# Kernel tuning notes

Measured on AMD Instinct MI355X. Metric: run time of the kernel, lower is better.

Reference implementation:

```python
import jax, jax.numpy as jnp
import numpy as np

N = 100000       # nodes
E = 1600000      # edges (avg degree 16)
W_IN = 256
W_HID = 64
T = 4            # node types
K = 10           # diffusion hops (num_layers)
ALPHA = 0.1
EPS = 1e-12


def setup_inputs() -> dict:
    key = jax.random.key(0)
    k1, k2, k3, k4, k5 = jax.random.split(key, 5)
    X = jax.random.normal(k1, (N, W_IN), dtype=jnp.float32)
    W_enc = jax.random.normal(k2, (W_IN, W_HID), dtype=jnp.float32) * 0.1  # xavier-ish scale
    b_enc = jnp.zeros((W_HID,), dtype=jnp.float32)
    gaussian_sample = jax.random.normal(k3, (N * W_HID,), dtype=jnp.float32)
    edge_index = jax.random.randint(k4, (2, E), 0, N, dtype=jnp.int64)
    node_type = jax.random.randint(k5, (N,), 0, T, dtype=jnp.int64)
    return {"X": X, "W_enc": W_enc, "b_enc": b_enc,
            "gaussian_sample": gaussian_sample,
            "edge_index": edge_index, "node_type": node_type}


def _l2_normalize_rows(x):
    # F.normalize(x, p=2, dim=1)
    n = jnp.sqrt(jnp.sum(x * x, axis=1, keepdims=True))
    return x / jnp.maximum(n, EPS)


def reference(X, W_enc, b_enc, gaussian_sample, edge_index, node_type):
    # --- type-aware encoding: Linear + L2 row-normalize (act='l2') ---
    H = X @ W_enc + b_enc                       # [N, W_HID]
    H = _l2_normalize_rows(H)

    # --- per-type statistics (vectorized segment reduce over node types) ---
    counts = jax.ops.segment_sum(jnp.ones((N,), H.dtype), node_type, num_segments=T)  # [T]
    mean_t = jax.ops.segment_sum(H, node_type, num_segments=T) / counts[:, None]      # [T, W_HID]
    dev2 = (H - mean_t[node_type]) ** 2
    # original: 1/sqrt(n_i - 1) * sum((H_i - mean_i)^2)  (sum, not mean — faithful)
    std_t = jax.ops.segment_sum(dev2, node_type, num_segments=T) / jnp.sqrt(counts - 1.0)[:, None]

    tilde_H = (H - mean_t[node_type]) / std_t[node_type]  # [N, W_HID]

    # --- wasserstein loss: W1 between flattened embeddings and a standard gaussian
    # sample of equal size (scipy wasserstein_distance == mean |sorted diffs|).
    # Original detaches embeddings (numpy), so stop_gradient the whole loss.
    emb = jax.lax.stop_gradient(tilde_H).reshape(-1)
    loss = jax.lax.stop_gradient(
        jnp.mean(jnp.abs(jnp.sort(gaussian_sample) - jnp.sort(emb))))

    # dropout with training=False -> identity

    # --- PPR diffusion: K steps of row-normalized SpMM with restart ---
    src, dst = edge_index[0], edge_index[1]
    deg = jax.ops.segment_sum(jnp.ones((E,), H.dtype), dst, num_segments=N)
    deg = jnp.maximum(deg, 1.0)                 # avoid div-by-zero for isolated nodes
    edge_norm = (1.0 / deg)[dst]                # D^{-1} A (row normalization)

    Z = tilde_H
    for _ in range(K):
        agg = jax.ops.segment_sum(Z[src] * edge_norm[:, None], dst, num_segments=N)
        Z = (1.0 - ALPHA) * agg + ALPHA * tilde_H

    # --- de-normalize back with per-type stats, then L2 row-normalize ---
    Z = Z * std_t[node_type] + mean_t[node_type]
    Z = _l2_normalize_rows(Z)
    return (Z, loss)
```

## Files before the change

### kernel.cpp

```cpp
#include <hip/hip_runtime.h>
#include <math.h>

#define WH 64
#define WIN 256
#define TT 4
#define ALPHA_C 0.1f
#define STATS_GRID 256
#define KC 32
#define ENC_T 64
#define ENC_BN 32
#define XTS 36
#define BINS 16384
#define BIN_SCALE 1024.0f
#define HG 256
#define SB 128
#define ST 256

typedef unsigned short ushortT;

__device__ __forceinline__ unsigned pack_bf16(float a, float b) {
  unsigned ua = __float_as_uint(a), ub = __float_as_uint(b);
  ua = (ua + 0x7FFFu + ((ua >> 16) & 1u)) >> 16;
  ub = ((ub + 0x7FFFu + ((ub >> 16) & 1u)) >> 16) << 16;
  return (ua & 0xFFFFu) | ub;
}
__device__ __forceinline__ float bf_lo(unsigned p) { return __uint_as_float(p << 16); }
__device__ __forceinline__ float bf_hi(unsigned p) { return __uint_as_float(p & 0xFFFF0000u); }

__global__ __launch_bounds__(64, 3) void k_encode(const float* __restrict__ X,
                                                  const float* __restrict__ W,
                                                  const float* __restrict__ bias,
                                                  float* __restrict__ H, int N) {
  __shared__ __align__(16) float XsT[KC * XTS];
  __shared__ __align__(16) float Ws[KC * WH];
  int tid = threadIdx.x;
  int ng = tid >> 3, cg = tid & 7;
  int nodeBase = blockIdx.x * ENC_BN;
  float acc[4][8] = {};
  for (int k0 = 0; k0 < WIN; k0 += KC) {
    __syncthreads();
    const float4* Wg4 = (const float4*)(W + (size_t)k0 * WH);
    float4* Ws4 = (float4*)Ws;
#pragma unroll
    for (int j = 0; j < 8; ++j) Ws4[tid + j * 64] = Wg4[tid + j * 64];
#pragma unroll
    for (int i = 0; i < 4; ++i) {
      int idx = tid + i * 64;
      int ln = idx >> 3, f4 = idx & 7;
      int node = nodeBase + ln;
      float4 xv = (node < N)
                      ? *(const float4*)(X + (size_t)node * WIN + k0 + f4 * 4)
                      : make_float4(0.f, 0.f, 0.f, 0.f);
      float* p = &XsT[(f4 * 4) * XTS + ln];
      p[0] = xv.x;
      p[XTS] = xv.y;
      p[2 * XTS] = xv.z;
      p[3 * XTS] = xv.w;
    }
    __syncthreads();
#pragma unroll 8
    for (int k = 0; k < KC; ++k) {
      float4 a0 = *(const float4*)&XsT[k * XTS + ng * 4];
      float4 b0 = *(const float4*)&Ws[k * WH + cg * 8];
      float4 b1 = *(const float4*)&Ws[k * WH + cg * 8 + 4];
      float av[4] = {a0.x, a0.y, a0.z, a0.w};
      float bb[8] = {b0.x, b0.y, b0.z, b0.w, b1.x, b1.y, b1.z, b1.w};
#pragma unroll
      for (int i = 0; i < 4; ++i)
#pragma unroll
        for (int j = 0; j < 8; ++j) acc[i][j] += av[i] * bb[j];
    }
  }
  float4 bb0 = *(const float4*)(bias + cg * 8);
  float4 bb1 = *(const float4*)(bias + cg * 8 + 4);
  float bv[8] = {bb0.x, bb0.y, bb0.z, bb0.w, bb1.x, bb1.y, bb1.z, bb1.w};
#pragma unroll
  for (int i = 0; i < 4; ++i) {
    float h[8];
    float s = 0.f;
#pragma unroll
    for (int j = 0; j < 8; ++j) {
      h[j] = acc[i][j] + bv[j];
      s += h[j] * h[j];
    }
    s += __shfl_xor(s, 1, 64);
    s += __shfl_xor(s, 2, 64);
    s += __shfl_xor(s, 4, 64);
    float r = 1.0f / fmaxf(sqrtf(s), 1e-12f);
    int node = nodeBase + ng * 4 + i;
    if (node < N) {
      float4 o0 = {h[0] * r, h[1] * r, h[2] * r, h[3] * r};
      float4 o1 = {h[4] * r, h[5] * r, h[6] * r, h[7] * r};
      *(float4*)(H + (size_t)node * WH + cg * 8) = o0;
      *(float4*)(H + (size_t)node * WH + cg * 8 + 4) = o1;
    }
  }
}

__global__ __launch_bounds__(256) void k_stats(const float* __restrict__ H,
                                               const int* __restrict__ nt,
                                               float* __restrict__ psum,
                                               float* __restrict__ psq,
                                               float* __restrict__ pcnt, int NW) {
  __shared__ float ls[TT * WH], ls2[TT * WH];
  __shared__ float lc[TT];
  ls[threadIdx.x] = 0.0f;
  ls2[threadIdx.x] = 0.0f;
  if (threadIdx.x < TT) lc[threadIdx.x] = 0.0f;
  __syncthreads();
  for (int i = blockIdx.x * 256 + threadIdx.x; i < NW; i += STATS_GRID * 256) {
    int nn = i >> 6, d = i & 63;
    int t = nt[nn];
    float v = H[i];
    atomicAdd(&ls[t * WH + d], v);
    atomicAdd(&ls2[t * WH + d], v * v);
    if (d == 0) atomicAdd(&lc[t], 1.0f);
  }
  __syncthreads();
  psum[blockIdx.x * 256 + threadIdx.x] = ls[threadIdx.x];
  psq[blockIdx.x * 256 + threadIdx.x] = ls2[threadIdx.x];
  if (threadIdx.x < TT) pcnt[blockIdx.x * TT + threadIdx.x] = lc[threadIdx.x];
}

__global__ __launch_bounds__(256) void k_reduce_stats(const float* __restrict__ psum,
                                                      const float* __restrict__ psq,
                                                      const float* __restrict__ pcnt,
                                                      float* __restrict__ mean,
                                                      float* __restrict__ stdv,
                                                      float* __restrict__ counts) {
  __shared__ float c[TT];
  if (threadIdx.x < TT) {
    float s = 0.0f;
    for (int b = 0; b < STATS_GRID; ++b) s += pcnt[b * TT + threadIdx.x];
    counts[threadIdx.x] = s;
    c[threadIdx.x] = s;
  }
  __syncthreads();
  float s = 0.0f, q = 0.0f;
  for (int b = 0; b < STATS_GRID; ++b) {
    s += psum[b * 256 + threadIdx.x];
    q += psq[b * 256 + threadIdx.x];
  }
  float n = c[threadIdx.x >> 6];
  float m = s / n;
  mean[threadIdx.x] = m;
  stdv[threadIdx.x] = (q - s * s / n) / sqrtf(n - 1.0f);
}

__global__ __launch_bounds__(256) void k_tilde_hist(float* __restrict__ H,
                                                    const int* __restrict__ nt,
                                                    const float* __restrict__ mean,
                                                    const float* __restrict__ stdv,
                                                    ushortT* __restrict__ tb,
                                                    unsigned* __restrict__ pe, int NW) {
  __shared__ unsigned hist[BINS];
  for (int b = threadIdx.x; b < BINS; b += 256) hist[b] = 0;
  __syncthreads();
  for (int i = blockIdx.x * 256 + threadIdx.x; i < NW; i += HG * 256) {
    int nn = i >> 6, d = i & 63;
    int t = nt[nn];
    float v = (H[i] - mean[t * WH + d]) / stdv[t * WH + d];
    H[i] = v;
    unsigned u = __float_as_uint(v);
    tb[i] = (ushortT)((u + 0x7FFFu + ((u >> 16) & 1u)) >> 16);
    int b = (int)((v + 8.0f) * BIN_SCALE);
    b = min(max(b, 0), BINS - 1);
    atomicAdd(&hist[b], 1u);
  }
  __syncthreads();
  for (int b = threadIdx.x; b < BINS; b += 256)
    pe[(size_t)blockIdx.x * BINS + b] = hist[b];
}

__global__ __launch_bounds__(256) void k_histG(const float* __restrict__ g,
                                               unsigned* __restrict__ pg, int M) {
  __shared__ unsigned hist[BINS];
  for (int b = threadIdx.x; b < BINS; b += 256) hist[b] = 0;
  __syncthreads();
  for (int i = blockIdx.x * 256 + threadIdx.x; i < M; i += HG * 256) {
    float v = g[i];
    int b = (int)((v + 8.0f) * BIN_SCALE);
    b = min(max(b, 0), BINS - 1);
    atomicAdd(&hist[b], 1u);
  }
  __syncthreads();
  for (int b = threadIdx.x; b < BINS; b += 256)
    pg[(size_t)blockIdx.x * BINS + b] = hist[b];
}

__global__ __launch_bounds__(256) void k_diff(const unsigned* __restrict__ pg,
                                              const unsigned* __restrict__ pe,
                                              int* __restrict__ diff) {
  int b = blockIdx.x * 256 + threadIdx.x;
  int s = 0;
  for (int p = 0; p < HG; ++p)
    s += (int)pg[(size_t)p * BINS + b] - (int)pe[(size_t)p * BINS + b];
  diff[b] = s;
}

__global__ __launch_bounds__(1024) void k_wass(const int* __restrict__ diff,
                                               float* __restrict__ out, int M, int NW) {
  int tid = threadIdx.x;
  int lo = tid * (BINS / 1024);
  int d[BINS / 1024];
  int s = 0;
#pragma unroll
  for (int i = 0; i < BINS / 1024; ++i) {
    d[i] = diff[lo + i];
    s += d[i];
  }
  __shared__ int sc[1024];
  sc[tid] = s;
  __syncthreads();
  for (int st = 1; st < 1024; st <<= 1) {
    int v = (tid >= st) ? sc[tid - st] : 0;
    __syncthreads();
    sc[tid] += v;
    __syncthreads();
  }
  int run = sc[tid] - s;
  long long a = 0;
#pragma unroll
  for (int i = 0; i < BINS / 1024; ++i) {
    run += d[i];
    a += (long long)(run < 0 ? -run : run);
  }
  __shared__ long long rd[1024];
  rd[tid] = a;
  __syncthreads();
  for (int st = 512; st > 0; st >>= 1) {
    if (tid < st) rd[tid] += rd[tid + st];
    __syncthreads();
  }
  if (tid == 0) out[NW] = (float)((double)rd[0] * (1.0 / (double)BIN_SCALE) / (double)M);
}

__global__ __launch_bounds__(256) void k_degi(const int* __restrict__ dst,
                                              unsigned* __restrict__ degi, int E) {
  int e = blockIdx.x * 256 + threadIdx.x;
  if (e < E) atomicAdd(&degi[dst[e]], 1u);
}

__global__ __launch_bounds__(ST) void k_scan_part(const unsigned* __restrict__ in,
                                                  unsigned* __restrict__ bsum, int L) {
  int C = (L + SB * ST - 1) / (SB * ST);
  int base = (blockIdx.x * ST + threadIdx.x) * C;
  int hi = min(base + C, L);
  unsigned s = 0;
  for (int i = base; i < hi; ++i) s += in[i];
  __shared__ unsigned red[ST];
  red[threadIdx.x] = s;
  __syncthreads();
  for (int st = ST / 2; st > 0; st >>= 1) {
    if (threadIdx.x < st) red[threadIdx.x] += red[threadIdx.x + st];
    __syncthreads();
  }
  if (threadIdx.x == 0) bsum[blockIdx.x] = red[0];
}
__global__ __launch_bounds__(ST) void k_scan_mid(unsigned* __restrict__ bsum) {
  __shared__ unsigned ts[ST];
  unsigned v = (threadIdx.x < SB) ? bsum[threadIdx.x] : 0u;
  ts[threadIdx.x] = v;
  __syncthreads();
  for (int st = 1; st < ST; st <<= 1) {
    unsigned u = (threadIdx.x >= (unsigned)st) ? ts[threadIdx.x - st] : 0u;
    __syncthreads();
    ts[threadIdx.x] += u;
    __syncthreads();
  }
  if (threadIdx.x < SB) bsum[threadIdx.x] = ts[threadIdx.x] - v;
}
__global__ __launch_bounds__(ST) void k_scan_apply(const unsigned* __restrict__ in,
                                                   const unsigned* __restrict__ bsum,
                                                   unsigned* __restrict__ outp, int L) {
  int C = (L + SB * ST - 1) / (SB * ST);
  int base = (blockIdx.x * ST + threadIdx.x) * C;
  int hi = min(base + C, L);
  unsigned s = 0;
  for (int i = base; i < hi; ++i) s += in[i];
  __shared__ unsigned ts[ST];
  ts[threadIdx.x] = s;
  __syncthreads();
  for (int st = 1; st < ST; st <<= 1) {
    unsigned u = (threadIdx.x >= (unsigned)st) ? ts[threadIdx.x - st] : 0u;
    __syncthreads();
    ts[threadIdx.x] += u;
    __syncthreads();
  }
  unsigned run = bsum[blockIdx.x] + ts[threadIdx.x] - s;
  for (int i = base; i < hi; ++i) {
    unsigned c = in[i];
    outp[i] = run;
    run += c;
  }
}

__global__ __launch_bounds__(256) void k_build(const int* __restrict__ src,
                                               const int* __restrict__ dst,
                                               const unsigned* __restrict__ off,
                                               unsigned* __restrict__ cur,
                                               unsigned* __restrict__ esrc, int E) {
  int e = blockIdx.x * 256 + threadIdx.x;
  if (e >= E) return;
  int t = dst[e];
  unsigned p = off[t] + atomicAdd(&cur[t], 1u);
  esrc[p] = (unsigned)src[e];
}

__global__ __launch_bounds__(256) void k_spmm(const unsigned* __restrict__ off,
                                              const unsigned* __restrict__ degi,
                                              const unsigned* __restrict__ esrc,
                                              const ushortT* __restrict__ Zb,
                                              const float* __restrict__ tilde,
                                              ushortT* __restrict__ Zn,
                                              const int* __restrict__ nt,
                                              const float* __restrict__ mean,
                                              const float* __restrict__ stdv,
                                              float* __restrict__ outp,
                                              int fin, int N) {
  int lane = threadIdx.x & 63, wv = threadIdx.x >> 6;
  int j = lane >> 3, c = lane & 7;
  int n = blockIdx.x * 32 + wv * 8 + j;
  if (n >= N) return;
  unsigned st = off[n], dg = degi[n];
  const unsigned* ep = esrc + st;
  float a[8] = {};
  unsigned e = 0;
  for (; e + 4 <= dg; e += 4) {
    unsigned s0 = ep[e], s1 = ep[e + 1], s2 = ep[e + 2], s3 = ep[e + 3];
    uint4 v0 = *((const uint4*)(Zb + (size_t)s0 * WH) + c);
    uint4 v1 = *((const uint4*)(Zb + (size_t)s1 * WH) + c);
    uint4 v2 = *((const uint4*)(Zb + (size_t)s2 * WH) + c);
    uint4 v3 = *((const uint4*)(Zb + (size_t)s3 * WH) + c);
    a[0] += bf_lo(v0.x) + bf_lo(v1.x) + bf_lo(v2.x) + bf_lo(v3.x);
    a[1] += bf_hi(v0.x) + bf_hi(v1.x) + bf_hi(v2.x) + bf_hi(v3.x);
    a[2] += bf_lo(v0.y) + bf_lo(v1.y) + bf_lo(v2.y) + bf_lo(v3.y);
    a[3] += bf_hi(v0.y) + bf_hi(v1.y) + bf_hi(v2.y) + bf_hi(v3.y);
    a[4] += bf_lo(v0.z) + bf_lo(v1.z) + bf_lo(v2.z) + bf_lo(v3.z);
    a[5] += bf_hi(v0.z) + bf_hi(v1.z) + bf_hi(v2.z) + bf_hi(v3.z);
    a[6] += bf_lo(v0.w) + bf_lo(v1.w) + bf_lo(v2.w) + bf_lo(v3.w);
    a[7] += bf_hi(v0.w) + bf_hi(v1.w) + bf_hi(v2.w) + bf_hi(v3.w);
  }
  for (; e < dg; ++e) {
    unsigned s = ep[e];
    uint4 v = *((const uint4*)(Zb + (size_t)s * WH) + c);
    a[0] += bf_lo(v.x); a[1] += bf_hi(v.x);
    a[2] += bf_lo(v.y); a[3] += bf_hi(v.y);
    a[4] += bf_lo(v.z); a[5] += bf_hi(v.z);
    a[6] += bf_lo(v.w); a[7] += bf_hi(v.w);
  }
  float wn = (1.0f - ALPHA_C) / fmaxf((float)dg, 1.0f);
  const float4* Tr = (const float4*)(tilde + (size_t)n * WH);
  float4 t0 = Tr[2 * c], t1 = Tr[2 * c + 1];
  float o0 = wn * a[0] + ALPHA_C * t0.x, o1 = wn * a[1] + ALPHA_C * t0.y;
  float o2 = wn * a[2] + ALPHA_C * t0.z, o3 = wn * a[3] + ALPHA_C * t0.w;
  float o4 = wn * a[4] + ALPHA_C * t1.x, o5 = wn * a[5] + ALPHA_C * t1.y;
  float o6 = wn * a[6] + ALPHA_C * t1.z, o7 = wn * a[7] + ALPHA_C * t1.w;
  if (!fin) {
    uint4 p;
    p.x = pack_bf16(o0, o1);
    p.y = pack_bf16(o2, o3);
    p.z = pack_bf16(o4, o5);
    p.w = pack_bf16(o6, o7);
    *((uint4*)(Zn + (size_t)n * WH) + c) = p;
  } else {
    int t = nt[n];
    float4 m0 = *(const float4*)(mean + t * WH + c * 8);
    float4 m1 = *(const float4*)(mean + t * WH + c * 8 + 4);
    float4 d0 = *(const float4*)(stdv + t * WH + c * 8);
    float4 d1 = *(const float4*)(stdv + t * WH + c * 8 + 4);
    float z0 = o0 * d0.x + m0.x, z1 = o1 * d0.y + m0.y;
    float z2 = o2 * d0.z + m0.z, z3 = o3 * d0.w + m0.w;
    float z4 = o4 * d1.x + m1.x, z5 = o5 * d1.y + m1.y;
    float z6 = o6 * d1.z + m1.z, z7 = o7 * d1.w + m1.w;
    float s = z0 * z0 + z1 * z1 + z2 * z2 + z3 * z3 +
              z4 * z4 + z5 * z5 + z6 * z6 + z7 * z7;
    s += __shfl_xor(s, 1, 64);
    s += __shfl_xor(s, 2, 64);
    s += __shfl_xor(s, 4, 64);
    float r = 1.0f / fmaxf(sqrtf(s), 1e-12f);
    float4 w0 = {z0 * r, z1 * r, z2 * r, z3 * r};
    float4 w1 = {z4 * r, z5 * r, z6 * r, z7 * r};
    *(float4*)(outp + (size_t)n * WH + c * 8) = w0;
    *(float4*)(outp + (size_t)n * WH + c * 8 + 4) = w1;
  }
}

extern "C" void kernel_launch(void* const* d_in, const int* in_sizes, int n_in,
                              void* d_out, int out_size, void* d_ws, size_t ws_size,
                              hipStream_t stream) {
  const float* X = (const float*)d_in[0];
  const float* W = (const float*)d_in[1];
  const float* bias = (const float*)d_in[2];
  const float* g = (const float*)d_in[3];
  const int* ei = (const int*)d_in[4];
  const int* nt = (const int*)d_in[5];

  const int N = in_sizes[5];
  const int E = in_sizes[4] / 2;
  const int M = in_sizes[3];
  const int NW = N * WH;
  const int* srcp = ei;
  const int* dstp = ei + E;

  char* w = (char*)d_ws;
  size_t o = 0;
  auto alloc = [&](size_t bytes) {
    size_t r = o;
    o += (bytes + 255) & ~(size_t)255;
    return r;
  };
  size_t off_stats = alloc(4096);
  size_t off_psum  = alloc((size_t)STATS_GRID * 256 * 4);
  size_t off_psq   = alloc((size_t)STATS_GRID * 256 * 4);
  size_t off_pcnt  = alloc((size_t)STATS_GRID * TT * 4);
  size_t off_diff  = alloc((size_t)BINS * 4);
  size_t off_bsum  = alloc((size_t)SB * 4);
  size_t off_degi  = alloc((size_t)N * 4);
  size_t off_cur   = alloc((size_t)N * 4);
  size_t off_off   = alloc((size_t)N * 4);
  size_t off_esrc  = alloc((size_t)E * 4);
  size_t off_tilde = alloc((size_t)NW * 4);
  size_t off_tbf   = alloc((size_t)NW * 2);
  size_t off_bufA  = alloc((size_t)NW * 4);
  size_t off_bufB  = alloc((size_t)NW * 4);

  float* counts = (float*)(w + off_stats + 0);
  float* mean   = (float*)(w + off_stats + 256);
  float* stdv   = (float*)(w + off_stats + 1280);
  float* psum   = (float*)(w + off_psum);
  float* psq    = (float*)(w + off_psq);
  float* pcnt   = (float*)(w + off_pcnt);
  int* diff     = (int*)(w + off_diff);
  unsigned* bsum = (unsigned*)(w + off_bsum);
  unsigned* degi = (unsigned*)(w + off_degi);
  unsigned* cur  = (unsigned*)(w + off_cur);
  unsigned* offp = (unsigned*)(w + off_off);
  unsigned* esrc = (unsigned*)(w + off_esrc);
  float* tilde   = (float*)(w + off_tilde);
  ushortT* tbf   = (ushortT*)(w + off_tbf);
  unsigned* pg   = (unsigned*)(w + off_bufA);
  unsigned* pe   = (unsigned*)(w + off_bufB);
  ushortT* ZA    = (ushortT*)(w + off_bufA);
  ushortT* ZB    = (ushortT*)(w + off_bufB);
  float* out = (float*)d_out;

  hipMemsetAsync(w + off_degi, 0, off_cur - off_degi + (size_t)N * 4, stream);

  k_encode<<<(N + ENC_BN - 1) / ENC_BN, ENC_T, 0, stream>>>(X, W, bias, tilde, N);

  k_stats<<<STATS_GRID, 256, 0, stream>>>(tilde, nt, psum, psq, pcnt, NW);
  k_reduce_stats<<<1, 256, 0, stream>>>(psum, psq, pcnt, mean, stdv, counts);

  k_tilde_hist<<<HG, 256, 0, stream>>>(tilde, nt, mean, stdv, tbf, pe, NW);
  k_histG<<<HG, 256, 0, stream>>>(g, pg, M);

  k_diff<<<BINS / 256, 256, 0, stream>>>(pg, pe, diff);
  k_wass<<<1, 1024, 0, stream>>>(diff, out, M, NW);

  k_degi<<<(E + 255) / 256, 256, 0, stream>>>(dstp, degi, E);
  k_scan_part<<<SB, ST, 0, stream>>>(degi, bsum, N);
  k_scan_mid<<<1, ST, 0, stream>>>(bsum);
  k_scan_apply<<<SB, ST, 0, stream>>>(degi, bsum, offp, N);
  k_build<<<(E + 255) / 256, 256, 0, stream>>>(srcp, dstp, offp, cur, esrc, E);

  const ushortT* Zc = tbf;
  for (int k = 0; k < 10; ++k) {
    ushortT* Zn = (k & 1) ? ZB : ZA;
    int fin = (k == 9) ? 1 : 0;
    k_spmm<<<(N + 31) / 32, 256, 0, stream>>>(offp, degi, esrc, Zc, tilde, Zn,
                                              nt, mean, stdv, out, fin, N);
    Zc = Zn;
  }
}
```

Measured before the change: 898.7 us.

## Fuse diffusion hops into one cooperative persistent kernel with grid sync

Replaces the ten per-hop SpMM launches with a single cooperative kernel that keeps per-node offsets, degrees and restart features in registers across hops and separates hops with grid.sync. Each thread covers up to four nodes in a strided persistent layout, aiming to remove launch overhead and repeated loads of node metadata. CSR construction also records each edge's rank from the degree-counting atomic, so the build pass needs no second atomic or cursor array. The risks are grid-wide barrier cost, lower occupancy from the fixed 1024x256 grid, and a fallback to the old path if the cooperative launch fails.

```diff
diff --git a/kernel.cpp b/kernel.cpp
--- a/kernel.cpp
+++ b/kernel.cpp
@@ -1,5 +1,8 @@
 #include <hip/hip_runtime.h>
+#include <hip/hip_cooperative_groups.h>
 #include <math.h>
+
+namespace cg = cooperative_groups;
 
 #define WH 64
 #define WIN 256
@@ -15,6 +18,9 @@
 #define HG 256
 #define SB 128
 #define ST 256
+#define HOP_B 1024
+#define HOP_T 256
+#define HOP_S ((HOP_B * HOP_T) / 8)
 
 typedef unsigned short ushortT;
 
@@ -34,7 +40,7 @@
   __shared__ __align__(16) float XsT[KC * XTS];
   __shared__ __align__(16) float Ws[KC * WH];
   int tid = threadIdx.x;
-  int ng = tid >> 3, cg = tid & 7;
+  int ng = tid >> 3, cg_ = tid & 7;
   int nodeBase = blockIdx.x * ENC_BN;
   float acc[4][8] = {};
   for (int k0 = 0; k0 < WIN; k0 += KC) {
@@ -61,8 +67,8 @@
 #pragma unroll 8
     for (int k = 0; k < KC; ++k) {
       float4 a0 = *(const float4*)&XsT[k * XTS + ng * 4];
-      float4 b0 = *(const float4*)&Ws[k * WH + cg * 8];
-      float4 b1 = *(const float4*)&Ws[k * WH + cg * 8 + 4];
+      float4 b0 = *(const float4*)&Ws[k * WH + cg_ * 8];
+      float4 b1 = *(const float4*)&Ws[k * WH + cg_ * 8 + 4];
       float av[4] = {a0.x, a0.y, a0.z, a0.w};
       float bb[8] = {b0.x, b0.y, b0.z, b0.w, b1.x, b1.y, b1.z, b1.w};
 #pragma unroll
@@ -71,8 +77,8 @@
         for (int j = 0; j < 8; ++j) acc[i][j] += av[i] * bb[j];
     }
   }
-  float4 bb0 = *(const float4*)(bias + cg * 8);
-  float4 bb1 = *(const float4*)(bias + cg * 8 + 4);
+  float4 bb0 = *(const float4*)(bias + cg_ * 8);
+  float4 bb1 = *(const float4*)(bias + cg_ * 8 + 4);
   float bv[8] = {bb0.x, bb0.y, bb0.z, bb0.w, bb1.x, bb1.y, bb1.z, bb1.w};
 #pragma unroll
   for (int i = 0; i < 4; ++i) {
@@ -91,8 +97,8 @@
     if (node < N) {
       float4 o0 = {h[0] * r, h[1] * r, h[2] * r, h[3] * r};
       float4 o1 = {h[4] * r, h[5] * r, h[6] * r, h[7] * r};
-      *(float4*)(H + (size_t)node * WH + cg * 8) = o0;
-      *(float4*)(H + (size_t)node * WH + cg * 8 + 4) = o1;
+      *(float4*)(H + (size_t)node * WH + cg_ * 8) = o0;
+      *(float4*)(H + (size_t)node * WH + cg_ * 8 + 4) = o1;
     }
   }
 }
@@ -235,10 +241,21 @@
   if (tid == 0) out[NW] = (float)((double)rd[0] * (1.0 / (double)BIN_SCALE) / (double)M);
 }
 
-__global__ __launch_bounds__(256) void k_degi(const int* __restrict__ dst,
-                                              unsigned* __restrict__ degi, int E) {
+__global__ __launch_bounds__(256) void k_degi_rank(const int* __restrict__ dst,
+                                                   unsigned* __restrict__ degi,
+                                                   unsigned* __restrict__ rank, int E) {
   int e = blockIdx.x * 256 + threadIdx.x;
-  if (e < E) atomicAdd(&degi[dst[e]], 1u);
+  if (e < E) rank[e] = atomicAdd(&degi[dst[e]], 1u);
+}
+
+__global__ __launch_bounds__(256) void k_build2(const int* __restrict__ src,
+                                                const int* __restrict__ dst,
+                                                const unsigned* __restrict__ off,
+                                                const unsigned* __restrict__ rank,
+                                                unsigned* __restrict__ esrc, int E) {
+  int e = blockIdx.x * 256 + threadIdx.x;
+  if (e >= E) return;
+  esrc[off[dst[e]] + rank[e]] = (unsigned)src[e];
 }
 
 __global__ __launch_bounds__(ST) void k_scan_part(const unsigned* __restrict__ in,
@@ -295,16 +312,111 @@
   }
 }
 
-__global__ __launch_bounds__(256) void k_build(const int* __restrict__ src,
-                                               const int* __restrict__ dst,
-                                               const unsigned* __restrict__ off,
-                                               unsigned* __restrict__ cur,
-                                               unsigned* __restrict__ esrc, int E) {
-  int e = blockIdx.x * 256 + threadIdx.x;
-  if (e >= E) return;
-  int t = dst[e];
-  unsigned p = off[t] + atomicAdd(&cur[t], 1u);
-  esrc[p] = (unsigned)src[e];
+__global__ __launch_bounds__(HOP_T, 4) void k_hops(
+    const unsigned* __restrict__ off, const unsigned* __restrict__ degi,
+    const unsigned* __restrict__ esrc, const ushortT* __restrict__ Z0,
+    const float* __restrict__ tilde, ushortT* __restrict__ ZAp,
+    ushortT* __restrict__ ZBp, const int* __restrict__ nt,
+    const float* __restrict__ mean, const float* __restrict__ stdv,
+    float* __restrict__ outp, int N, int K) {
+  cg::grid_group grid = cg::this_grid();
+  int g = blockIdx.x * HOP_T + threadIdx.x;
+  int slot = g >> 3, c = g & 7;
+  unsigned stv[4], dgv[4];
+  float4 tA[4], tB[4];
+  int nn[4];
+#pragma unroll
+  for (int i = 0; i < 4; ++i) {
+    int n = slot + i * HOP_S;
+    nn[i] = -1;
+    stv[i] = 0; dgv[i] = 0;
+    tA[i] = make_float4(0.f, 0.f, 0.f, 0.f);
+    tB[i] = make_float4(0.f, 0.f, 0.f, 0.f);
+    if (n < N) {
+      nn[i] = n;
+      stv[i] = off[n];
+      dgv[i] = degi[n];
+      const float4* Tr = (const float4*)(tilde + (size_t)n * WH);
+      tA[i] = Tr[2 * c];
+      tB[i] = Tr[2 * c + 1];
+    }
+  }
+  const ushortT* Zb = Z0;
+  ushortT* Zn = ZAp;
+  for (int k = 0; k < K; ++k) {
+    int fin = (k == K - 1);
+#pragma unroll
+    for (int i = 0; i < 4; ++i) {
+      if (nn[i] < 0) break;
+      int n = nn[i];
+      const unsigned* ep = esrc + stv[i];
+      unsigned dg = dgv[i];
+      float a[8] = {};
+      unsigned e = 0;
+      for (; e + 4 <= dg; e += 4) {
+        unsigned s0 = ep[e], s1 = ep[e + 1], s2 = ep[e + 2], s3 = ep[e + 3];
+        uint4 v0 = *((const uint4*)(Zb + (size_t)s0 * WH) + c);
+        uint4 v1 = *((const uint4*)(Zb + (size_t)s1 * WH) + c);
+        uint4 v2 = *((const uint4*)(Zb + (size_t)s2 * WH) + c);
+        uint4 v3 = *((const uint4*)(Zb + (size_t)s3 * WH) + c);
+        a[0] += bf_lo(v0.x) + bf_lo(v1.x) + bf_lo(v2.x) + bf_lo(v3.x);
+        a[1] += bf_hi(v0.x) + bf_hi(v1.x) + bf_hi(v2.x) + bf_hi(v3.x);
+        a[2] += bf_lo(v0.y) + bf_lo(v1.y) + bf_lo(v2.y) + bf_lo(v3.y);
+        a[3] += bf_hi(v0.y) + bf_hi(v1.y) + bf_hi(v2.y) + bf_hi(v3.y);
+        a[4] += bf_lo(v0.z) + bf_lo(v1.z) + bf_lo(v2.z) + bf_lo(v3.z);
+        a[5] += bf_hi(v0.z) + bf_hi(v1.z) + bf_hi(v2.z) + bf_hi(v3.z);
+        a[6] += bf_lo(v0.w) + bf_lo(v1.w) + bf_lo(v2.w) + bf_lo(v3.w);
+        a[7] += bf_hi(v0.w) + bf_hi(v1.w) + bf_hi(v2.w) + bf_hi(v3.w);
+      }
+      for (; e < dg; ++e) {
+        unsigned s = ep[e];
+        uint4 v = *((const uint4*)(Zb + (size_t)s * WH) + c);
+        a[0] += bf_lo(v.x); a[1] += bf_hi(v.x);
+        a[2] += bf_lo(v.y); a[3] += bf_hi(v.y);
+        a[4] += bf_lo(v.z); a[5] += bf_hi(v.z);
+        a[6] += bf_lo(v.w); a[7] += bf_hi(v.w);
+      }
+      float wn = (1.0f - ALPHA_C) / fmaxf((float)dg, 1.0f);
+      float o0 = wn * a[0] + ALPHA_C * tA[i].x, o1 = wn * a[1] + ALPHA_C * tA[i].y;
+      float o2 = wn * a[2] + ALPHA_C * tA[i].z, o3 = wn * a[3] + ALPHA_C * tA[i].w;
+      float o4 = wn * a[4] + ALPHA_C * tB[i].x, o5 = wn * a[5] + ALPHA_C * tB[i].y;
+      float o6 = wn * a[6] + ALPHA_C * tB[i].z, o7 = wn * a[7] + ALPHA_C * tB[i].w;
+      if (!fin) {
+        uint4 p;
+        p.x = pack_bf16(o0, o1);
+        p.y = pack_bf16(o2, o3);
+        p.z = pack_bf16(o4, o5);
+        p.w = pack_bf16(o6, o7);
+        *((uint4*)(Zn + (size_t)n * WH) + c) = p;
+      } else {
+        int t = nt[n];
+        float4 m0 = *(const float4*)(mean + t * WH + c * 8);
+        float4 m1 = *(const float4*)(mean + t * WH + c * 8 + 4);
+        float4 d0 = *(const float4*)(stdv + t * WH + c * 8);
+        float4 d1 = *(const float4*)(stdv + t * WH + c * 8 + 4);
+        float z0 = o0 * d0.x + m0.x, z1 = o1 * d0.y + m0.y;
+        float z2 = o2 * d0.z + m0.z, z3 = o3 * d0.w + m0.w;
+        float z4 = o4 * d1.x + m1.x, z5 = o5 * d1.y + m1.y;
+        float z6 = o6 * d1.z + m1.z, z7 = o7 * d1.w + m1.w;
+        float s = z0 * z0 + z1 * z1 + z2 * z2 + z3 * z3 +
+                  z4 * z4 + z5 * z5 + z6 * z6 + z7 * z7;
+        s += __shfl_xor(s, 1, 64);
+        s += __shfl_xor(s, 2, 64);
+        s += __shfl_xor(s, 4, 64);
+        float r = 1.0f / fmaxf(sqrtf(s), 1e-12f);
+        float4 w0 = {z0 * r, z1 * r, z2 * r, z3 * r};
+        float4 w1 = {z4 * r, z5 * r, z6 * r, z7 * r};
+        *(float4*)(outp + (size_t)n * WH + c * 8) = w0;
+        *(float4*)(outp + (size_t)n * WH + c * 8 + 4) = w1;
+      }
+    }
+    if (k < K - 1) {
+      __threadfence();
+      grid.sync();
+      Zb = Zn;
+      Zn = (Zn == ZAp) ? ZBp : ZAp;
+    }
+  }
 }
 
 __global__ __launch_bounds__(256) void k_spmm(const unsigned* __restrict__ off,
@@ -417,7 +529,6 @@
   size_t off_diff  = alloc((size_t)BINS * 4);
   size_t off_bsum  = alloc((size_t)SB * 4);
   size_t off_degi  = alloc((size_t)N * 4);
-  size_t off_cur   = alloc((size_t)N * 4);
   size_t off_off   = alloc((size_t)N * 4);
   size_t off_esrc  = alloc((size_t)E * 4);
   size_t off_tilde = alloc((size_t)NW * 4);
@@ -434,18 +545,18 @@
   int* diff     = (int*)(w + off_diff);
   unsigned* bsum = (unsigned*)(w + off_bsum);
   unsigned* degi = (unsigned*)(w + off_degi);
-  unsigned* cur  = (unsigned*)(w + off_cur);
   unsigned* offp = (unsigned*)(w + off_off);
   unsigned* esrc = (unsigned*)(w + off_esrc);
   float* tilde   = (float*)(w + off_tilde);
   ushortT* tbf   = (ushortT*)(w + off_tbf);
   unsigned* pg   = (unsigned*)(w + off_bufA);
   unsigned* pe   = (unsigned*)(w + off_bufB);
+  unsigned* rank = (unsigned*)(w + off_bufB);
   ushortT* ZA    = (ushortT*)(w + off_bufA);
   ushortT* ZB    = (ushortT*)(w + off_bufB);
   float* out = (float*)d_out;
 
-  hipMemsetAsync(w + off_degi, 0, off_cur - off_degi + (size_t)N * 4, stream);
+  hipMemsetAsync(w + off_degi, 0, (size_t)N * 4, stream);
 
   k_encode<<<(N + ENC_BN - 1) / ENC_BN, ENC_T, 0, stream>>>(X, W, bias, tilde, N);
 
@@ -458,18 +569,31 @@
   k_diff<<<BINS / 256, 256, 0, stream>>>(pg, pe, diff);
   k_wass<<<1, 1024, 0, stream>>>(diff, out, M, NW);
 
-  k_degi<<<(E + 255) / 256, 256, 0, stream>>>(dstp, degi, E);
+  k_degi_rank<<<(E + 255) / 256, 256, 0, stream>>>(dstp, degi, rank, E);
   k_scan_part<<<SB, ST, 0, stream>>>(degi, bsum, N);
   k_scan_mid<<<1, ST, 0, stream>>>(bsum);
   k_scan_apply<<<SB, ST, 0, stream>>>(degi, bsum, offp, N);
-  k_build<<<(E + 255) / 256, 256, 0, stream>>>(srcp, dstp, offp, cur, esrc, E);
-
-  const ushortT* Zc = tbf;
-  for (int k = 0; k < 10; ++k) {
-    ushortT* Zn = (k & 1) ? ZB : ZA;
-    int fin = (k == 9) ? 1 : 0;
-    k_spmm<<<(N + 31) / 32, 256, 0, stream>>>(offp, degi, esrc, Zc, tilde, Zn,
-                                              nt, mean, stdv, out, fin, N);
-    Zc = Zn;
-  }
-}
+  k_build2<<<(E + 255) / 256, 256, 0, stream>>>(srcp, dstp, offp, rank, esrc, E);
+
+  hipError_t cerr = hipErrorUnknown;
+  if ((N + HOP_S - 1) / HOP_S <= 4) {
+    const ushortT* Z0 = tbf;
+    int K = 10;
+    void* args[] = {(void*)&offp, (void*)&degi, (void*)&esrc, (void*)&Z0,
+                    (void*)&tilde, (void*)&ZA, (void*)&ZB, (void*)&nt,
+                    (void*)&mean, (void*)&stdv, (void*)&out, (void*)&N, (void*)&K};
+    cerr = hipLaunchCooperativeKernel(reinterpret_cast<void*>(k_hops),
+                                      dim3(HOP_B), dim3(HOP_T), args, 0, stream);
+  }
+  if (cerr != hipSuccess) {
+    (void)hipGetLastError();
+    const ushortT* Zc = tbf;
+    for (int k = 0; k < 10; ++k) {
+      ushortT* Zn = (k & 1) ? ZB : ZA;
+      int fin = (k == 9) ? 1 : 0;
+      k_spmm<<<(N + 31) / 32, 256, 0, stream>>>(offp, degi, esrc, Zc, tilde, Zn,
+                                                nt, mean, stdv, out, fin, N);
+      Zc = Zn;
+    }
+  }
+}
```

After: 2.838 ms. +215.8%, slower.
